# Performance work log

Measured on AMD Instinct MI355X. Metric: run time of the kernel, lower is better.

Reference implementation:

```python
import jax, jax.numpy as jnp
import numpy as np

N_NODES = 100_000
N_EDGES = 500_000
G = 1024          # num_graphs
H = 128           # hidden_dim
S_PER = 4         # start nodes per graph
EPS_LN = 1e-5


def _ln(x, g, b):
    m = x.mean(-1, keepdims=True)
    v = ((x - m) ** 2).mean(-1, keepdims=True)
    return (x - m) / jnp.sqrt(v + EPS_LN) * g + b


def _gelu(x):
    return jax.nn.gelu(x, approximate=False)  # torch nn.GELU default (erf)


def setup_inputs() -> dict:
    key = jax.random.key(0)
    ks = jax.random.split(key, 24)
    S = G * S_PER
    d = {
        'node_tokens': jax.random.normal(ks[0], (N_NODES, H), jnp.float32),
        'question_tokens': jax.random.normal(ks[1], (G, H), jnp.float32),
        'edge_tokens': jax.random.normal(ks[2], (N_EDGES, H), jnp.float32),
        'start_node_locals': jax.random.randint(ks[3], (S,), 0, N_NODES),
        'start_node_ptr': jnp.arange(G + 1) * S_PER,
        'edge_batch': jnp.sort(jax.random.randint(ks[4], (N_EDGES,), 0, G)),
        'selected_mask': jax.random.bernoulli(ks[5], 0.5, (N_EDGES,)),
        'edge_index': jax.random.randint(ks[6], (2, N_EDGES), 0, N_NODES),
    }
    w = lambda k, shp: jax.random.normal(k, shp, jnp.float32) * 0.02
    # log_z_head: LN(H) -> Linear(H,H) -> GELU -> Linear(H,1)
    d['ln1_g'] = jnp.ones((H,)); d['ln1_b'] = jnp.zeros((H,))
    d['zw1'] = w(ks[7], (H, H)); d['zb1'] = w(ks[8], (H,))
    d['zw2'] = w(ks[9], (H, 1)); d['zb2'] = jnp.zeros((1,))
    # ctx_projector: Linear(2H,H) -> GELU -> Linear(H,H)
    d['cw1'] = w(ks[10], (2 * H, H)); d['cb1'] = w(ks[11], (H,))
    d['cw2'] = w(ks[12], (H, H)); d['cb2'] = w(ks[13], (H,))
    # backward_head: LN(3H) -> Linear(3H,H) -> GELU -> (Dropout: identity in eval) -> Linear(H,1)
    d['bln_g'] = jnp.ones((3 * H,)); d['bln_b'] = jnp.zeros((3 * H,))
    d['bw1'] = w(ks[14], (3 * H, H)); d['bb1'] = w(ks[15], (H,))
    d['bw2'] = w(ks[16], (H, 1)); d['bb2'] = jnp.zeros((1,))
    return d


def reference(node_tokens, question_tokens, edge_tokens,
              ln1_g, ln1_b, zw1, zb1, zw2, zb2,
              cw1, cb1, cw2, cb2,
              bln_g, bln_b, bw1, bb1, bw2, bb2,
              start_node_locals, start_node_ptr, edge_batch, selected_mask, edge_index):
    counts = start_node_ptr[1:] - start_node_ptr[:-1]                       # [G]
    batch_index = jnp.repeat(jnp.arange(G), counts, total_repeat_length=start_node_locals.shape[0])
    # --- aggregate_start: gather + segment softmax + scatter-add ---
    start_tokens = node_tokens[start_node_locals]                            # [S,H]
    q = question_tokens[batch_index]                                         # [S,H]
    scores = (start_tokens * q).sum(-1) / jnp.sqrt(jnp.float32(H))           # [S]
    m = jax.ops.segment_max(scores, batch_index, num_segments=G)             # [G]
    ex = jnp.exp(scores - m[batch_index])
    denom = jax.ops.segment_sum(ex, batch_index, num_segments=G)
    alpha = ex / denom[batch_index]                                          # pyg_softmax (eps-free path)
    summary = jax.ops.segment_sum(start_tokens * alpha[:, None], batch_index, num_segments=G)  # [G,H]
    # --- build_context + log_z ---
    ctx_in = jnp.concatenate([summary, question_tokens], axis=-1)            # [G,2H]
    context = _gelu(ctx_in @ cw1 + cb1) @ cw2 + cb2                          # [G,H]
    log_z = (_gelu(_ln(context, ln1_g, ln1_b) @ zw1 + zb1) @ zw2 + zb2)[:, 0]  # [G]
    # --- log_pb (learned): gather + segment log-softmax over target nodes + scatter-add per graph ---
    tgt = edge_index[1]                                                      # [E]
    tail = node_tokens[tgt]                                                  # [E,H]
    edge_ctx = jnp.concatenate([edge_tokens, question_tokens[edge_batch], tail], axis=-1)  # [E,3H]
    logits = (_gelu(_ln(edge_ctx, bln_g, bln_b) @ bw1 + bb1) @ bw2 + bb2)[:, 0]            # [E]
    tmax = jax.ops.segment_max(logits, tgt, num_segments=N_NODES)
    shifted = logits - tmax[tgt]
    lse = jnp.log(jax.ops.segment_sum(jnp.exp(shifted), tgt, num_segments=N_NODES))
    log_probs = shifted - lse[tgt]                                           # scatter_log_softmax
    sel = selected_mask.astype(logits.dtype)
    log_pb_per_graph = jax.ops.segment_sum(log_probs * sel, edge_batch, num_segments=G)    # [G]
    # pb_nll: masked mean over graphs that have a selected edge
    nll_per_graph = jax.ops.segment_sum(-log_probs * sel, edge_batch, num_segments=G)
    has_edge = jax.ops.segment_sum(sel, edge_batch, num_segments=G) > 0
    pb_nll = jnp.where(has_edge, nll_per_graph, 0.0).sum() / jnp.maximum(has_edge.sum(), 1).astype(logits.dtype)
    return jnp.stack([log_z, log_pb_per_graph, jnp.broadcast_to(pb_nll, log_z.shape)], axis=-1)  # [G,3]
```

## Files before the change

kernel.cpp:

```cpp
#include <hip/hip_runtime.h>
#include <math.h>

#define G_NUM 1024
#define H 128
#define NNODES 100000
#define NEDGES 500000
#define EPS_LN 1e-5f

typedef __attribute__((ext_vector_type(8))) short short8;
typedef __attribute__((ext_vector_type(4))) float f32x4;

__device__ __forceinline__ float gelu_exact(float x) {
    return 0.5f * x * (1.0f + erff(x * 0.70710678118654752440f));
}
__device__ __forceinline__ unsigned short f2bf(float x) {
    unsigned u = __float_as_uint(x);
    return (unsigned short)((u + 0x7FFFu + ((u >> 16) & 1u)) >> 16);
}

__global__ void k_probe_mask(const unsigned* __restrict__ mw, int* __restrict__ flag) {
    unsigned v = mw[threadIdx.x];
    if (v == 0x3F800000u) atomicOr(flag, 2);
    else if (v > 1u) atomicOr(flag, 1);
}

__global__ void k_prep(const float* __restrict__ bw1, const float* __restrict__ blng,
                       unsigned short* __restrict__ bwbf) {
    int e = blockIdx.x * 256 + threadIdx.x;
    if (e >= 384 * 128) return;
    int k = e >> 7, n = e & 127;
    int s = k >> 5, krel = k & 31;
    int quad = krel >> 3, j = krel & 7;
    int lane = quad * 16 + (n & 15);
    int t8 = n >> 4;
    bwbf[((s * 8 + t8) * 64 + lane) * 8 + j] = f2bf(bw1[e] * blng[k]);
}

__global__ __launch_bounds__(128) void k_prep2(const float* __restrict__ bw1,
                                               const float* __restrict__ blng,
                                               const float* __restrict__ blnb,
                                               const float* __restrict__ bb1,
                                               float* __restrict__ colsum,
                                               float* __restrict__ bb1p) {
    int n = threadIdx.x;
    float cs = 0.f, bs = 0.f;
    for (int k = 0; k < 384; ++k) {
        float w = bw1[k * H + n];
        cs += blng[k] * w;
        bs += blnb[k] * w;
    }
    colsum[n] = cs;
    bb1p[n] = bb1[n] + bs;
}

__global__ __launch_bounds__(128) void k_graph(
    const float* __restrict__ node_tokens, const float* __restrict__ question,
    const int* __restrict__ locals_, const int* __restrict__ ptr,
    const float* __restrict__ cw1, const float* __restrict__ cb1,
    const float* __restrict__ cw2, const float* __restrict__ cb2,
    const float* __restrict__ ln1g, const float* __restrict__ ln1b,
    const float* __restrict__ zw1, const float* __restrict__ zb1,
    const float* __restrict__ zw2, const float* __restrict__ zb2,
    float* __restrict__ out)
{
    int g = blockIdx.x, t = threadIdx.x;
    __shared__ float xin[2 * H];
    __shared__ float buf[H];
    __shared__ float r1[2], r2[2];
    __shared__ float sc[16];
    int p0 = ptr[g], p1 = ptr[g + 1];
    int cnt = p1 - p0; if (cnt > 16) cnt = 16;
    float q = question[(size_t)g * H + t];
    xin[H + t] = q;
    for (int s = 0; s < cnt; ++s) {
        int node = locals_[p0 + s];
        float v = node_tokens[(size_t)node * H + t] * q;
        for (int off = 32; off; off >>= 1) v += __shfl_down(v, off);
        if ((t & 63) == 0) r1[t >> 6] = v;
        __syncthreads();
        if (t == 0) sc[s] = (r1[0] + r1[1]) * 0.08838834764831845f;
        __syncthreads();
    }
    float m = -1e30f;
    for (int s = 0; s < cnt; ++s) m = fmaxf(m, sc[s]);
    float den = 0.f;
    for (int s = 0; s < cnt; ++s) den += expf(sc[s] - m);
    float acc0 = 0.f;
    for (int s = 0; s < cnt; ++s) {
        float a = expf(sc[s] - m) / den;
        acc0 += a * node_tokens[(size_t)locals_[p0 + s] * H + t];
    }
    xin[t] = acc0;
    __syncthreads();
    float a1 = cb1[t];
    for (int k = 0; k < 2 * H; ++k) a1 += xin[k] * cw1[k * H + t];
    buf[t] = gelu_exact(a1);
    __syncthreads();
    float ctx = cb2[t];
    for (int k = 0; k < H; ++k) ctx += buf[k] * cw2[k * H + t];
    float s1 = ctx, s2 = ctx * ctx;
    for (int off = 32; off; off >>= 1) { s1 += __shfl_down(s1, off); s2 += __shfl_down(s2, off); }
    if ((t & 63) == 0) { r1[t >> 6] = s1; r2[t >> 6] = s2; }
    __syncthreads();
    float mean = (r1[0] + r1[1]) * (1.f / H);
    float var  = (r2[0] + r2[1]) * (1.f / H) - mean * mean;
    float xn = (ctx - mean) * rsqrtf(var + EPS_LN) * ln1g[t] + ln1b[t];
    __syncthreads();
    buf[t] = xn;
    __syncthreads();
    float a2 = zb1[t];
    for (int k = 0; k < H; ++k) a2 += buf[k] * zw1[k * H + t];
    float p = gelu_exact(a2) * zw2[t];
    for (int off = 32; off; off >>= 1) p += __shfl_down(p, off);
    if ((t & 63) == 0) r1[t >> 6] = p;
    __syncthreads();
    if (t == 0) out[(size_t)g * 3 + 0] = r1[0] + r1[1] + zb2[0];
}

__global__ __launch_bounds__(256) void k_edges(
    const float* __restrict__ node_tokens, const float* __restrict__ question,
    const float* __restrict__ edge_tokens, const int* __restrict__ edge_batch,
    const int* __restrict__ edge_index,
    const unsigned short* __restrict__ bwbf, const float* __restrict__ colsum,
    const float* __restrict__ bb1p, const float* __restrict__ bw2,
    const float* __restrict__ bb2, float* __restrict__ logits,
    float* __restrict__ sumexp)
{
    __shared__ unsigned short bstage[4096];
    int t = threadIdx.x, lane = t & 63, w = t >> 6;
    int quad = lane >> 4, n16 = lane & 15;
    int e0 = blockIdx.x * 64;
    int e = e0 + w * 16 + n16;
    int ec = e < NEDGES ? e : NEDGES - 1;
    int qrow = edge_batch[ec];
    int trow = edge_index[NEDGES + ec];
    const float4* ep = (const float4*)(edge_tokens + (size_t)ec * H);
    const float4* qp = (const float4*)(question + (size_t)qrow * H);
    const float4* np_ = (const float4*)(node_tokens + (size_t)trow * H);

    float s1 = 0.f, s2 = 0.f;
    short8 frag[12];
    #pragma unroll
    for (int s = 0; s < 12; ++s) {
        int c0 = s * 8 + quad * 2;
        const float4* base = (s < 4) ? ep : (s < 8) ? qp : np_;
        int cc = c0 - ((s < 4) ? 0 : (s < 8) ? 32 : 64);
        float4 v0 = base[cc], v1 = base[cc + 1];
        s1 += v0.x + v0.y + v0.z + v0.w + v1.x + v1.y + v1.z + v1.w;
        s2 += v0.x*v0.x + v0.y*v0.y + v0.z*v0.z + v0.w*v0.w
            + v1.x*v1.x + v1.y*v1.y + v1.z*v1.z + v1.w*v1.w;
        short8 f;
        f[0] = (short)f2bf(v0.x); f[1] = (short)f2bf(v0.y);
        f[2] = (short)f2bf(v0.z); f[3] = (short)f2bf(v0.w);
        f[4] = (short)f2bf(v1.x); f[5] = (short)f2bf(v1.y);
        f[6] = (short)f2bf(v1.z); f[7] = (short)f2bf(v1.w);
        frag[s] = f;
    }
    s1 += __shfl_xor(s1, 16); s1 += __shfl_xor(s1, 32);
    s2 += __shfl_xor(s2, 16); s2 += __shfl_xor(s2, 32);
    float mu  = s1 * (1.f / 384.f);
    float inv = rsqrtf(s2 * (1.f / 384.f) - mu * mu + EPS_LN);

    f32x4 acc[8];
    #pragma unroll
    for (int q = 0; q < 8; ++q) acc[q] = (f32x4){0.f, 0.f, 0.f, 0.f};

    #pragma unroll
    for (int s = 0; s < 12; ++s) {
        __syncthreads();
        {
            const uint4* src = (const uint4*)(bwbf + s * 4096);
            uint4* dst = (uint4*)bstage;
            dst[t] = src[t];
            dst[t + 256] = src[t + 256];
        }
        __syncthreads();
        #pragma unroll
        for (int t8 = 0; t8 < 8; ++t8) {
            short8 b = *(const short8*)&bstage[(t8 * 64 + lane) * 8];
            acc[t8] = __builtin_amdgcn_mfma_f32_16x16x32_bf16(frag[s], b, acc[t8], 0, 0, 0);
        }
    }

    float csv[8], bbv[8], w2v[8];
    #pragma unroll
    for (int t8 = 0; t8 < 8; ++t8) {
        int n = t8 * 16 + n16;
        csv[t8] = colsum[n]; bbv[t8] = bb1p[n]; w2v[t8] = bw2[n];
    }
    float bb2v = bb2[0];
    #pragma unroll
    for (int r = 0; r < 4; ++r) {
        float mu_r  = __shfl(mu,  quad * 4 + r);
        float inv_r = __shfl(inv, quad * 4 + r);
        float ssum = 0.f;
        #pragma unroll
        for (int t8 = 0; t8 < 8; ++t8) {
            float y = (acc[t8][r] - mu_r * csv[t8]) * inv_r + bbv[t8];
            ssum += gelu_exact(y) * w2v[t8];
        }
        ssum += __shfl_xor(ssum, 1);
        ssum += __shfl_xor(ssum, 2);
        ssum += __shfl_xor(ssum, 4);
        ssum += __shfl_xor(ssum, 8);
        if (n16 == 0) {
            int ei = e0 + w * 16 + quad * 4 + r;
            if (ei < NEDGES) {
                float lg = ssum + bb2v;
                logits[ei] = lg;
                atomicAdd(&sumexp[edge_index[NEDGES + ei]], expf(lg));
            }
        }
    }
}

__global__ __launch_bounds__(256) void k_logpb(
    const float* __restrict__ logits,
    const int* __restrict__ edge_index,
    const int* __restrict__ edge_batch,
    const void* __restrict__ mask,
    const int* __restrict__ flag,
    const float* __restrict__ sumexp,
    float* __restrict__ logpb, int* __restrict__ selcnt)
{
    __shared__ float lacc[8];
    __shared__ int lcnt[8];
    __shared__ int g0s, big;
    int t = threadIdx.x;
    int e0 = blockIdx.x * 256;
    if (t == 0) {
        int ga = edge_batch[e0 < NEDGES ? e0 : NEDGES - 1];
        int el = e0 + 255; if (el >= NEDGES) el = NEDGES - 1;
        int gb = edge_batch[el];
        g0s = ga; big = (gb - ga > 7);
    }
    if (t < 8) { lacc[t] = 0.f; lcnt[t] = 0; }
    __syncthreads();
    int e = e0 + t;
    if (e < NEDGES) {
        int mode = *flag;
        bool sel;
        if (mode & 2)      sel = ((const float*)mask)[e] != 0.f;
        else if (mode & 1) sel = ((const unsigned char*)mask)[e] != 0;
        else               sel = ((const int*)mask)[e] != 0;
        if (sel) {
            int tg = edge_index[NEDGES + e];
            float lp = logits[e] - logf(sumexp[tg]);
            int g = edge_batch[e];
            if (!big) {
                atomicAdd(&lacc[g - g0s], lp);
                atomicAdd(&lcnt[g - g0s], 1);
            } else {
                atomicAdd(&logpb[g], lp);
                atomicAdd(&selcnt[g], 1);
            }
        }
    }
    __syncthreads();
    if (t < 8 && !big && lcnt[t] > 0) {
        atomicAdd(&logpb[g0s + t], lacc[t]);
        atomicAdd(&selcnt[g0s + t], lcnt[t]);
    }
}

__global__ __launch_bounds__(1024) void k_final(const float* __restrict__ logpb,
                                                const int* __restrict__ selcnt,
                                                float* __restrict__ out)
{
    int g = threadIdx.x;
    float lpb = logpb[g];
    int has = selcnt[g] > 0;
    float s = has ? -lpb : 0.f;
    int c = has;
    __shared__ float rn[16];
    __shared__ int rh[16];
    __shared__ float pbnll_s;
    for (int off = 32; off; off >>= 1) { s += __shfl_down(s, off); c += __shfl_down(c, off); }
    if ((g & 63) == 0) { rn[g >> 6] = s; rh[g >> 6] = c; }
    __syncthreads();
    if (g == 0) {
        float ts = 0.f; int tc = 0;
        for (int i = 0; i < 16; ++i) { ts += rn[i]; tc += rh[i]; }
        pbnll_s = ts / (float)(tc > 0 ? tc : 1);
    }
    __syncthreads();
    out[(size_t)g * 3 + 1] = lpb;
    out[(size_t)g * 3 + 2] = pbnll_s;
}

extern "C" void kernel_launch(void* const* d_in, const int* in_sizes, int n_in,
                              void* d_out, int out_size, void* d_ws, size_t ws_size,
                              hipStream_t stream) {
    const float* node_tokens = (const float*)d_in[0];
    const float* question    = (const float*)d_in[1];
    const float* edge_tokens = (const float*)d_in[2];
    const int*   locals_     = (const int*)d_in[3];
    const int*   ptr         = (const int*)d_in[4];
    const int*   edge_batch  = (const int*)d_in[5];
    const void*  mask        = d_in[6];
    const int*   edge_index  = (const int*)d_in[7];
    const float* ln1g = (const float*)d_in[8];
    const float* ln1b = (const float*)d_in[9];
    const float* zw1  = (const float*)d_in[10];
    const float* zb1  = (const float*)d_in[11];
    const float* zw2  = (const float*)d_in[12];
    const float* zb2  = (const float*)d_in[13];
    const float* cw1  = (const float*)d_in[14];
    const float* cb1  = (const float*)d_in[15];
    const float* cw2  = (const float*)d_in[16];
    const float* cb2  = (const float*)d_in[17];
    const float* blng = (const float*)d_in[18];
    const float* blnb = (const float*)d_in[19];
    const float* bw1  = (const float*)d_in[20];
    const float* bb1  = (const float*)d_in[21];
    const float* bw2  = (const float*)d_in[22];
    const float* bb2  = (const float*)d_in[23];
    float* out = (float*)d_out;

    float* ws = (float*)d_ws;
    float* sumexp  = ws;
    float* logpb   = ws + 100000;
    int*   selcnt  = (int*)(ws + 101024);
    int*   flag    = (int*)(ws + 102048);
    float* logits  = ws + 102052;
    float* colsum  = ws + 602052;
    float* bb1p    = ws + 602180;
    unsigned short* bwbf = (unsigned short*)(ws + 602308);

    hipMemsetAsync(d_ws, 0, (size_t)102049 * 4, stream);
    k_probe_mask<<<1, 256, 0, stream>>>((const unsigned*)mask, flag);
    k_prep<<<192, 256, 0, stream>>>(bw1, blng, bwbf);
    k_prep2<<<1, 128, 0, stream>>>(bw1, blng, blnb, bb1, colsum, bb1p);
    k_graph<<<G_NUM, 128, 0, stream>>>(node_tokens, question, locals_, ptr,
                                       cw1, cb1, cw2, cb2, ln1g, ln1b,
                                       zw1, zb1, zw2, zb2, out);
    k_edges<<<(NEDGES + 63) / 64, 256, 0, stream>>>(node_tokens, question, edge_tokens,
                                                    edge_batch, edge_index, bwbf,
                                                    colsum, bb1p, bw2, bb2,
                                                    logits, sumexp);
    int eb = (NEDGES + 255) / 256;
    k_logpb<<<eb, 256, 0, stream>>>(logits, edge_index, edge_batch, mask, flag,
                                    sumexp, logpb, selcnt);
    k_final<<<1, 1024, 0, stream>>>(logpb, selcnt, out);
}
```

Measured before the change: 620.6 us.

## Make edge MLP kernel persistent with weights resident in LDS and merge setup kernels

Turns k_edges into a persistent grid of 256 blocks of 512 threads. Each block stages two thirds of the bf16 weight matrix into LDS once, and each wave processes 32-edge tiles as two 16-edge MFMA halves that share each weight fragment. The last third of the weights is read directly from global/L2. This removes the per-block reloading of the weights with its 12 barrier pairs and doubles MFMA reuse per B fragment, at the cost of higher register pressure, 64KB of LDS per block, and a fixed grid of only 256 blocks. The three small setup kernels are also merged into one launch, and bf16 packing switches to the hip_bf16 intrinsics.

```diff
diff --git a/kernel.cpp b/kernel.cpp
--- a/kernel.cpp
+++ b/kernel.cpp
@@ -1,4 +1,5 @@
 #include <hip/hip_runtime.h>
+#include <hip/hip_bf16.h>
 #include <math.h>
 
 #define G_NUM 1024
@@ -6,6 +7,7 @@
 #define NNODES 100000
 #define NEDGES 500000
 #define EPS_LN 1e-5f
+#define NTILES 15625
 
 typedef __attribute__((ext_vector_type(8))) short short8;
 typedef __attribute__((ext_vector_type(4))) float f32x4;
@@ -17,40 +19,47 @@
     unsigned u = __float_as_uint(x);
     return (unsigned short)((u + 0x7FFFu + ((u >> 16) & 1u)) >> 16);
 }
-
-__global__ void k_probe_mask(const unsigned* __restrict__ mw, int* __restrict__ flag) {
-    unsigned v = mw[threadIdx.x];
-    if (v == 0x3F800000u) atomicOr(flag, 2);
-    else if (v > 1u) atomicOr(flag, 1);
-}
-
-__global__ void k_prep(const float* __restrict__ bw1, const float* __restrict__ blng,
-                       unsigned short* __restrict__ bwbf) {
-    int e = blockIdx.x * 256 + threadIdx.x;
-    if (e >= 384 * 128) return;
-    int k = e >> 7, n = e & 127;
-    int s = k >> 5, krel = k & 31;
-    int quad = krel >> 3, j = krel & 7;
-    int lane = quad * 16 + (n & 15);
-    int t8 = n >> 4;
-    bwbf[((s * 8 + t8) * 64 + lane) * 8 + j] = f2bf(bw1[e] * blng[k]);
-}
-
-__global__ __launch_bounds__(128) void k_prep2(const float* __restrict__ bw1,
-                                               const float* __restrict__ blng,
-                                               const float* __restrict__ blnb,
-                                               const float* __restrict__ bb1,
-                                               float* __restrict__ colsum,
-                                               float* __restrict__ bb1p) {
-    int n = threadIdx.x;
-    float cs = 0.f, bs = 0.f;
-    for (int k = 0; k < 384; ++k) {
-        float w = bw1[k * H + n];
-        cs += blng[k] * w;
-        bs += blnb[k] * w;
-    }
-    colsum[n] = cs;
-    bb1p[n] = bb1[n] + bs;
+union BF8u { short8 s8; __hip_bfloat162 h[4]; };
+__device__ __forceinline__ short8 pack8(float4 a, float4 b) {
+    BF8u u;
+    u.h[0] = __float22bfloat162_rn(make_float2(a.x, a.y));
+    u.h[1] = __float22bfloat162_rn(make_float2(a.z, a.w));
+    u.h[2] = __float22bfloat162_rn(make_float2(b.x, b.y));
+    u.h[3] = __float22bfloat162_rn(make_float2(b.z, b.w));
+    return u.s8;
+}
+
+__global__ __launch_bounds__(256) void k_setup(
+    const unsigned* __restrict__ mw, int* __restrict__ flag,
+    const float* __restrict__ bw1, const float* __restrict__ blng,
+    const float* __restrict__ blnb, const float* __restrict__ bb1,
+    unsigned short* __restrict__ bwbf, float* __restrict__ colsum,
+    float* __restrict__ bb1p)
+{
+    int b = blockIdx.x, t = threadIdx.x;
+    if (b == 0) {
+        unsigned v = mw[t];
+        if (v == 0x3F800000u) atomicOr(flag, 2);
+        else if (v > 1u) atomicOr(flag, 1);
+    } else if (b <= 192) {
+        int e = (b - 1) * 256 + t;
+        int k = e >> 7, n = e & 127;
+        int s = k >> 5, krel = k & 31;
+        int quad = krel >> 3, j = krel & 7;
+        int lane = quad * 16 + (n & 15);
+        int t8 = n >> 4;
+        bwbf[((s * 8 + t8) * 64 + lane) * 8 + j] = f2bf(bw1[e] * blng[k]);
+    } else if (t < 128) {
+        int n = t;
+        float cs = 0.f, bs = 0.f;
+        for (int k = 0; k < 384; ++k) {
+            float w = bw1[k * H + n];
+            cs += blng[k] * w;
+            bs += blnb[k] * w;
+        }
+        colsum[n] = cs;
+        bb1p[n] = bb1[n] + bs;
+    }
 }
 
 __global__ __launch_bounds__(128) void k_graph(
@@ -117,7 +126,7 @@
     if (t == 0) out[(size_t)g * 3 + 0] = r1[0] + r1[1] + zb2[0];
 }
 
-__global__ __launch_bounds__(256) void k_edges(
+__global__ __launch_bounds__(512, 2) void k_edges(
     const float* __restrict__ node_tokens, const float* __restrict__ question,
     const float* __restrict__ edge_tokens, const int* __restrict__ edge_batch,
     const int* __restrict__ edge_index,
@@ -126,61 +135,19 @@
     const float* __restrict__ bb2, float* __restrict__ logits,
     float* __restrict__ sumexp)
 {
-    __shared__ unsigned short bstage[4096];
+    __shared__ unsigned short bsh[32768];
     int t = threadIdx.x, lane = t & 63, w = t >> 6;
     int quad = lane >> 4, n16 = lane & 15;
-    int e0 = blockIdx.x * 64;
-    int e = e0 + w * 16 + n16;
-    int ec = e < NEDGES ? e : NEDGES - 1;
-    int qrow = edge_batch[ec];
-    int trow = edge_index[NEDGES + ec];
-    const float4* ep = (const float4*)(edge_tokens + (size_t)ec * H);
-    const float4* qp = (const float4*)(question + (size_t)qrow * H);
-    const float4* np_ = (const float4*)(node_tokens + (size_t)trow * H);
-
-    float s1 = 0.f, s2 = 0.f;
-    short8 frag[12];
-    #pragma unroll
-    for (int s = 0; s < 12; ++s) {
-        int c0 = s * 8 + quad * 2;
-        const float4* base = (s < 4) ? ep : (s < 8) ? qp : np_;
-        int cc = c0 - ((s < 4) ? 0 : (s < 8) ? 32 : 64);
-        float4 v0 = base[cc], v1 = base[cc + 1];
-        s1 += v0.x + v0.y + v0.z + v0.w + v1.x + v1.y + v1.z + v1.w;
-        s2 += v0.x*v0.x + v0.y*v0.y + v0.z*v0.z + v0.w*v0.w
-            + v1.x*v1.x + v1.y*v1.y + v1.z*v1.z + v1.w*v1.w;
-        short8 f;
-        f[0] = (short)f2bf(v0.x); f[1] = (short)f2bf(v0.y);
-        f[2] = (short)f2bf(v0.z); f[3] = (short)f2bf(v0.w);
-        f[4] = (short)f2bf(v1.x); f[5] = (short)f2bf(v1.y);
-        f[6] = (short)f2bf(v1.z); f[7] = (short)f2bf(v1.w);
-        frag[s] = f;
-    }
-    s1 += __shfl_xor(s1, 16); s1 += __shfl_xor(s1, 32);
-    s2 += __shfl_xor(s2, 16); s2 += __shfl_xor(s2, 32);
-    float mu  = s1 * (1.f / 384.f);
-    float inv = rsqrtf(s2 * (1.f / 384.f) - mu * mu + EPS_LN);
-
-    f32x4 acc[8];
-    #pragma unroll
-    for (int q = 0; q < 8; ++q) acc[q] = (f32x4){0.f, 0.f, 0.f, 0.f};
-
-    #pragma unroll
-    for (int s = 0; s < 12; ++s) {
-        __syncthreads();
-        {
-            const uint4* src = (const uint4*)(bwbf + s * 4096);
-            uint4* dst = (uint4*)bstage;
-            dst[t] = src[t];
-            dst[t + 256] = src[t + 256];
-        }
-        __syncthreads();
+
+    {
+        const uint4* src = (const uint4*)bwbf;
+        uint4* dst = (uint4*)bsh;
         #pragma unroll
-        for (int t8 = 0; t8 < 8; ++t8) {
-            short8 b = *(const short8*)&bstage[(t8 * 64 + lane) * 8];
-            acc[t8] = __builtin_amdgcn_mfma_f32_16x16x32_bf16(frag[s], b, acc[t8], 0, 0, 0);
-        }
-    }
+        for (int i = 0; i < 8; ++i) dst[t + i * 512] = src[t + i * 512];
+    }
+    __syncthreads();
+
+    const short8* bglob = (const short8*)bwbf;
 
     float csv[8], bbv[8], w2v[8];
     #pragma unroll
@@ -189,26 +156,90 @@
         csv[t8] = colsum[n]; bbv[t8] = bb1p[n]; w2v[t8] = bw2[n];
     }
     float bb2v = bb2[0];
-    #pragma unroll
-    for (int r = 0; r < 4; ++r) {
-        float mu_r  = __shfl(mu,  quad * 4 + r);
-        float inv_r = __shfl(inv, quad * 4 + r);
-        float ssum = 0.f;
+
+    for (int it = 0; it < 8; ++it) {
+        int T = it * 2048 + blockIdx.x * 8 + w;
+        if (T >= NTILES) continue;
+        int ebase = T * 32;
+        int e0 = ebase + n16, e1 = ebase + 16 + n16;
+        int q0 = edge_batch[e0], q1 = edge_batch[e1];
+        int t0 = edge_index[NEDGES + e0], t1 = edge_index[NEDGES + e1];
+        const float4* eb0 = (const float4*)(edge_tokens + (size_t)e0 * H);
+        const float4* eb1 = (const float4*)(edge_tokens + (size_t)e1 * H);
+        const float4* qb0 = (const float4*)(question + (size_t)q0 * H);
+        const float4* qb1 = (const float4*)(question + (size_t)q1 * H);
+        const float4* nb0 = (const float4*)(node_tokens + (size_t)t0 * H);
+        const float4* nb1 = (const float4*)(node_tokens + (size_t)t1 * H);
+
+        float s1a = 0.f, s2a = 0.f, s1b = 0.f, s2b = 0.f;
+        f32x4 accA[8], accB[8];
         #pragma unroll
         for (int t8 = 0; t8 < 8; ++t8) {
-            float y = (acc[t8][r] - mu_r * csv[t8]) * inv_r + bbv[t8];
-            ssum += gelu_exact(y) * w2v[t8];
-        }
-        ssum += __shfl_xor(ssum, 1);
-        ssum += __shfl_xor(ssum, 2);
-        ssum += __shfl_xor(ssum, 4);
-        ssum += __shfl_xor(ssum, 8);
-        if (n16 == 0) {
-            int ei = e0 + w * 16 + quad * 4 + r;
-            if (ei < NEDGES) {
-                float lg = ssum + bb2v;
-                logits[ei] = lg;
-                atomicAdd(&sumexp[edge_index[NEDGES + ei]], expf(lg));
+            accA[t8] = (f32x4){0.f, 0.f, 0.f, 0.f};
+            accB[t8] = (f32x4){0.f, 0.f, 0.f, 0.f};
+        }
+
+        #pragma unroll
+        for (int s = 0; s < 12; ++s) {
+            int c = s * 8 + quad * 2;
+            const float4 *pa, *pb;
+            if (s < 4)      { pa = eb0 + c;        pb = eb1 + c; }
+            else if (s < 8) { pa = qb0 + (c - 32); pb = qb1 + (c - 32); }
+            else            { pa = nb0 + (c - 64); pb = nb1 + (c - 64); }
+            float4 a0 = pa[0], a1 = pa[1], b0 = pb[0], b1 = pb[1];
+            s1a += (a0.x + a0.y) + (a0.z + a0.w) + (a1.x + a1.y) + (a1.z + a1.w);
+            s2a += a0.x*a0.x + a0.y*a0.y + a0.z*a0.z + a0.w*a0.w
+                 + a1.x*a1.x + a1.y*a1.y + a1.z*a1.z + a1.w*a1.w;
+            s1b += (b0.x + b0.y) + (b0.z + b0.w) + (b1.x + b1.y) + (b1.z + b1.w);
+            s2b += b0.x*b0.x + b0.y*b0.y + b0.z*b0.z + b0.w*b0.w
+                 + b1.x*b1.x + b1.y*b1.y + b1.z*b1.z + b1.w*b1.w;
+            short8 fA = pack8(a0, a1), fB = pack8(b0, b1);
+            #pragma unroll
+            for (int t8 = 0; t8 < 8; ++t8) {
+                short8 bf;
+                if (s < 8) bf = *(const short8*)&bsh[((s * 8 + t8) * 64 + lane) * 8];
+                else       bf = bglob[(s * 8 + t8) * 64 + lane];
+                accA[t8] = __builtin_amdgcn_mfma_f32_16x16x32_bf16(fA, bf, accA[t8], 0, 0, 0);
+                accB[t8] = __builtin_amdgcn_mfma_f32_16x16x32_bf16(fB, bf, accB[t8], 0, 0, 0);
+            }
+        }
+
+        s1a += __shfl_xor(s1a, 16); s1a += __shfl_xor(s1a, 32);
+        s2a += __shfl_xor(s2a, 16); s2a += __shfl_xor(s2a, 32);
+        s1b += __shfl_xor(s1b, 16); s1b += __shfl_xor(s1b, 32);
+        s2b += __shfl_xor(s2b, 16); s2b += __shfl_xor(s2b, 32);
+        float muA = s1a * (1.f / 384.f);
+        float invA = rsqrtf(s2a * (1.f / 384.f) - muA * muA + EPS_LN);
+        float muB = s1b * (1.f / 384.f);
+        float invB = rsqrtf(s2b * (1.f / 384.f) - muB * muB + EPS_LN);
+
+        #pragma unroll
+        for (int h = 0; h < 2; ++h) {
+            float mu_h = h ? muB : muA, inv_h = h ? invB : invA;
+            int   tg_h = h ? t1 : t0;
+            #pragma unroll
+            for (int r = 0; r < 4; ++r) {
+                int src = quad * 4 + r;
+                float mu_r  = __shfl(mu_h, src);
+                float inv_r = __shfl(inv_h, src);
+                int   tg    = __shfl(tg_h, src);
+                float ssum = 0.f;
+                #pragma unroll
+                for (int t8 = 0; t8 < 8; ++t8) {
+                    float av = h ? accB[t8][r] : accA[t8][r];
+                    float y = (av - mu_r * csv[t8]) * inv_r + bbv[t8];
+                    ssum += gelu_exact(y) * w2v[t8];
+                }
+                ssum += __shfl_xor(ssum, 1);
+                ssum += __shfl_xor(ssum, 2);
+                ssum += __shfl_xor(ssum, 4);
+                ssum += __shfl_xor(ssum, 8);
+                if (n16 == 0) {
+                    int ei = ebase + h * 16 + quad * 4 + r;
+                    float lg = ssum + bb2v;
+                    logits[ei] = lg;
+                    atomicAdd(&sumexp[tg], expf(lg));
+                }
             }
         }
     }
@@ -328,16 +359,14 @@
     unsigned short* bwbf = (unsigned short*)(ws + 602308);
 
     hipMemsetAsync(d_ws, 0, (size_t)102049 * 4, stream);
-    k_probe_mask<<<1, 256, 0, stream>>>((const unsigned*)mask, flag);
-    k_prep<<<192, 256, 0, stream>>>(bw1, blng, bwbf);
-    k_prep2<<<1, 128, 0, stream>>>(bw1, blng, blnb, bb1, colsum, bb1p);
+    k_setup<<<194, 256, 0, stream>>>((const unsigned*)mask, flag, bw1, blng, blnb,
+                                     bb1, bwbf, colsum, bb1p);
     k_graph<<<G_NUM, 128, 0, stream>>>(node_tokens, question, locals_, ptr,
                                        cw1, cb1, cw2, cb2, ln1g, ln1b,
                                        zw1, zb1, zw2, zb2, out);
-    k_edges<<<(NEDGES + 63) / 64, 256, 0, stream>>>(node_tokens, question, edge_tokens,
-                                                    edge_batch, edge_index, bwbf,
-                                                    colsum, bb1p, bw2, bb2,
-                                                    logits, sumexp);
+    k_edges<<<256, 512, 0, stream>>>(node_tokens, question, edge_tokens,
+                                     edge_batch, edge_index, bwbf,
+                                     colsum, bb1p, bw2, bb2, logits, sumexp);
     int eb = (NEDGES + 255) / 256;
     k_logpb<<<eb, 256, 0, stream>>>(logits, edge_index, edge_batch, mask, flag,
                                     sumexp, logpb, selcnt);
```

Measured after the change: 815.9 us. 1.31x slower.
